# Performance work log

Hardware: AMD Instinct MI355X
Metric: run time of the kernel (lower is better)

Reference implementation:

```python
import jax, jax.numpy as jnp
import numpy as np

B, DIN, H, NACT = 8192, 1025, 1024, 1026
NHEAD = 513  # npatches + STOP
K = 32       # kR = kS


def _make_seq(key, batch, n, k):
    k_idx, k_len = jax.random.split(key)
    # distinct indices per row: top-k of a random permutation
    perm = jnp.argsort(jax.random.uniform(k_idx, (batch, n)), axis=1)[:, :k]
    seq_len = jax.random.randint(k_len, (batch,), 1, k + 1).astype(jnp.int32)
    mask = jnp.arange(k)[None, :] < seq_len[:, None]
    seq_idx = jnp.where(mask, perm, -1).astype(jnp.int32)
    return seq_idx, seq_len


def setup_inputs() -> dict:
    key = jax.random.key(0)
    ks = jax.random.split(key, 8)
    state = jax.random.normal(ks[0], (B, DIN), dtype=jnp.float32)
    W0 = jax.random.normal(ks[1], (DIN, H), dtype=jnp.float32) * (2.0 / DIN) ** 0.5
    b0 = jnp.zeros((H,), jnp.float32)
    W1 = jax.random.normal(ks[2], (H, H), dtype=jnp.float32) * (2.0 / H) ** 0.5
    b1 = jnp.zeros((H,), jnp.float32)
    W2 = jax.random.normal(ks[3], (H, NACT), dtype=jnp.float32) * 0.01
    b2 = jnp.zeros((NACT,), jnp.float32)
    seq_idx_R, seq_len_R = _make_seq(ks[4], B, NHEAD, K)
    seq_idx_S, seq_len_S = _make_seq(ks[5], B, NHEAD, K)
    return {"state": state, "W0": W0, "b0": b0, "W1": W1, "b1": b1,
            "W2": W2, "b2": b2,
            "seq_idx_R": seq_idx_R, "seq_len_R": seq_len_R,
            "seq_idx_S": seq_idx_S, "seq_len_S": seq_len_S}


def _mlp(state, W0, b0, W1, b1, W2, b2):
    h = jax.nn.relu(state @ W0 + b0)
    h = jax.nn.relu(h @ W1 + b1)
    return h @ W2 + b2  # (B, NACT) logits


def _logprob_entropy_wo_replacement(logits, seq_idx, seq_len):
    # Faithful vectorized version of logprob_entropy_wo_replacement_batched.
    bsz, n = logits.shape
    col = jnp.arange(n)[None, :]
    neg_inf = jnp.float32(-jnp.inf)

    def step(carry, xs):
        remaining, logp, ent = carry          # (B,N) bool, (B,), (B,)
        t, idx_t = xs                          # scalar, (B,)
        active = t < seq_len                   # (B,)
        masked_logits = jnp.where(remaining, logits, neg_inf)
        lp = jax.nn.log_softmax(masked_logits, axis=-1)
        p = jnp.exp(lp)
        mp = jnp.where(remaining, p, 0.0)
        mlp_ = jnp.where(remaining, lp, 0.0)
        ent_step = -jnp.sum(mp * mlp_, axis=-1)
        ent = ent + jnp.where(active, ent_step, 0.0)
        valid = active & (idx_t >= 0)
        idx_safe = jnp.where(valid, idx_t, 0)
        g = jnp.take_along_axis(lp, idx_safe[:, None], axis=1)[:, 0]
        logp = logp + jnp.where(valid, g, 0.0)
        hit = (col == idx_safe[:, None]) & valid[:, None]
        remaining = remaining & ~hit
        return (remaining, logp, ent), None

    init = (jnp.ones((bsz, n), bool), jnp.zeros((bsz,), jnp.float32),
            jnp.zeros((bsz,), jnp.float32))
    ts = jnp.arange(seq_idx.shape[1], dtype=jnp.int32)
    (_, logp, ent), _ = jax.lax.scan(step, init, (ts, seq_idx.T))
    return logp, ent


def reference(state, W0, b0, W1, b1, W2, b2,
              seq_idx_R, seq_len_R, seq_idx_S, seq_len_S):
    x = _mlp(state, W0, b0, W1, b1, W2, b2)
    logpR, entR = _logprob_entropy_wo_replacement(x[:, :NHEAD], seq_idx_R, seq_len_R)
    logpS, entS = _logprob_entropy_wo_replacement(x[:, NHEAD:NHEAD + NHEAD], seq_idx_S, seq_len_S)
    # rows: [total logprob, total entropy] as in get_log_prob's (logpR+logpS, entR+entS)
    return jnp.stack([logpR + logpS, entR + entS], axis=0)  # (2, B)
```

## Files before the change

### kernel.cpp

```cpp
#include <hip/hip_runtime.h>
#include <cstdint>
#include <cstddef>

#define BATCH 8192
#define DIN   1025
#define HID   1024
#define NACT  1026
#define NHEAD 513
#define KSEL  32
#define KP0   1088
#define LGN   1024

typedef unsigned short u16;
typedef short bf16x8 __attribute__((ext_vector_type(8)));
typedef float f32x4 __attribute__((ext_vector_type(4)));

__device__ __forceinline__ u16 f2bf(float f) {
  unsigned u = __float_as_uint(f);
  u += 0x7fff + ((u >> 16) & 1);
  return (u16)(u >> 16);
}
__device__ __forceinline__ float bf2f(u16 h) {
  return __uint_as_float((unsigned)h << 16);
}

__device__ __forceinline__ void async_cp16(const u16* g, u16* l) {
  __builtin_amdgcn_global_load_lds((const __attribute__((address_space(1))) void*)g,
                                   (__attribute__((address_space(3))) void*)l,
                                   16, 0, 0);
}

__global__ __launch_bounds__(512) void k_cvt(const float* __restrict__ state,
    const float* __restrict__ W0, const float* __restrict__ W1,
    const float* __restrict__ W2,
    u16* __restrict__ As, u16* __restrict__ W0t, u16* __restrict__ W1t,
    u16* __restrict__ W2t, u16* __restrict__ W2c) {
  const int tid = threadIdx.x;
  const int b = blockIdx.x;
  {
    int i = b * 512 + tid;
    const int QPR = KP0 / 4;
    int r = i / QPR, c4 = (i - r * QPR) * 4;
    const float* src = state + (size_t)r * DIN + c4;
    ushort4 o;
    if (c4 + 3 < DIN) {
      o.x = f2bf(src[0]); o.y = f2bf(src[1]); o.z = f2bf(src[2]); o.w = f2bf(src[3]);
    } else {
      o.x = (c4 + 0 < DIN) ? f2bf(src[0]) : 0;
      o.y = (c4 + 1 < DIN) ? f2bf(src[1]) : 0;
      o.z = (c4 + 2 < DIN) ? f2bf(src[2]) : 0;
      o.w = (c4 + 3 < DIN) ? f2bf(src[3]) : 0;
    }
    *(ushort4*)(As + (size_t)r * KP0 + c4) = o;
  }
  if (b >= 3137) return;
  if (b == 3136) {
    for (int e = tid; e < 2048; e += 512) {
      int j = e >> 10, k = e & 1023;
      W2c[e] = f2bf(W2[(size_t)k * NACT + 1024 + j]);
    }
    return;
  }
  const float* W; u16* Wt; int K, ldW, Kp, tt = b;
  if (tt < 1088)      { W = W0; Wt = W0t; K = DIN; ldW = HID;  Kp = KP0; }
  else if (tt < 2112) { tt -= 1088; W = W1; Wt = W1t; K = HID; ldW = HID;  Kp = HID; }
  else                { tt -= 2112; W = W2; Wt = W2t; K = HID; ldW = NACT; Kp = HID; }
  int n0 = (tt & 31) * 32, k0 = (tt >> 5) * 32;
  __shared__ float tile[32][33];
  const int tx = tid & 31, ty = tid >> 5;
#pragma unroll
  for (int i = 0; i < 32; i += 16) {
    int k = k0 + ty + i;
    tile[ty + i][tx] = (k < K) ? W[(size_t)k * ldW + n0 + tx] : 0.f;
  }
  __syncthreads();
#pragma unroll
  for (int i = 0; i < 32; i += 16)
    Wt[(size_t)(n0 + ty + i) * Kp + k0 + tx] = f2bf(tile[tx][ty + i]);
}

template<bool RELU, int K>
__global__ __launch_bounds__(512, 2)
void gemm256(const u16* __restrict__ A, const u16* __restrict__ Bt,
             const float* __restrict__ bias, u16* __restrict__ Cout, int ldc)
{
  __shared__ __align__(16) u16 lds[65536];

  const int d = blockIdx.x;
  const int wg    = (d & 7) * 16 + (d >> 3);
  const int mtile = wg >> 2;
  const int ntile = wg & 3;
  const size_t bm = (size_t)mtile * 256;
  const size_t bn = (size_t)ntile * 256;

  const int tid  = threadIdx.x;
  const int wave = tid >> 6;
  const int lane = tid & 63;
  const int waveM = wave >> 2, waveN = wave & 3;
  const int lr = lane & 15, lq = lane >> 4;
  const int xr = lr & 7;

  const int row0 = tid >> 3;
  const int g_   = (tid & 7) ^ ((tid >> 3) & 7);
  const u16* gA0 = A  + (bm + row0)       * (size_t)K + g_ * 8;
  const u16* gA1 = A  + (bm + row0 + 64)  * (size_t)K + g_ * 8;
  const u16* gA2 = A  + (bm + row0 + 128) * (size_t)K + g_ * 8;
  const u16* gA3 = A  + (bm + row0 + 192) * (size_t)K + g_ * 8;
  const u16* gB0 = Bt + (bn + row0)       * (size_t)K + g_ * 8;
  const u16* gB1 = Bt + (bn + row0 + 64)  * (size_t)K + g_ * 8;
  const u16* gB2 = Bt + (bn + row0 + 128) * (size_t)K + g_ * 8;
  const u16* gB3 = Bt + (bn + row0 + 192) * (size_t)K + g_ * 8;
  u16* lA = lds + wave * 512;
  u16* lB = lds + 16384 + wave * 512;

  const u16* paA = lds + (waveM * 128 + lr) * 64;
  const u16* paB = lds + 16384 + (waveN * 64 + lr) * 64;
  const int s0 = ( lq      ^ xr) * 8;
  const int s1 = ((4 | lq) ^ xr) * 8;

  f32x4 acc[8][4] = {};
  bf16x8 af[4], ag[4], bfr[4], bgr[4];

  {
    async_cp16(gA0, lA);            async_cp16(gA1, lA + 4096);
    async_cp16(gA2, lA + 8192);     async_cp16(gA3, lA + 12288);
    async_cp16(gB0, lB);            async_cp16(gB1, lB + 4096);
    async_cp16(gB2, lB + 8192);     async_cp16(gB3, lB + 12288);
    asm volatile("s_waitcnt vmcnt(0)" ::: "memory");
    __builtin_amdgcn_s_barrier();
  }

  const int NIT = K / 64;
#pragma unroll 2
  for (int it = 0; it < NIT; ++it) {
    const int bo  = (it & 1) ? 32768 : 0;
    const int bo2 = 32768 - bo;
    const int kn  = (it + 1) * 64;
    const bool pf = (it + 1 < NIT);

#pragma unroll
    for (int nf = 0; nf < 4; ++nf) bfr[nf] = *(const bf16x8*)(paB + bo + nf * 1024 + s0);
#pragma unroll
    for (int mf = 0; mf < 4; ++mf) af[mf]  = *(const bf16x8*)(paA + bo + mf * 1024 + s0);
    if (pf) {
      async_cp16(gA0 + kn, lA + bo2);         async_cp16(gA1 + kn, lA + bo2 + 4096);
      async_cp16(gA2 + kn, lA + bo2 + 8192);  async_cp16(gA3 + kn, lA + bo2 + 12288);
    }
    __builtin_amdgcn_s_barrier();
    asm volatile("s_waitcnt lgkmcnt(0)" ::: "memory");
    __builtin_amdgcn_sched_barrier(0);
    __builtin_amdgcn_s_setprio(1);
#pragma unroll
    for (int mf = 0; mf < 4; ++mf)
#pragma unroll
      for (int nf = 0; nf < 4; ++nf)
        acc[mf][nf] = __builtin_amdgcn_mfma_f32_16x16x32_bf16(af[mf], bfr[nf], acc[mf][nf], 0, 0, 0);
    __builtin_amdgcn_s_setprio(0);
    __builtin_amdgcn_s_barrier();

#pragma unroll
    for (int mf = 0; mf < 4; ++mf) ag[mf] = *(const bf16x8*)(paA + bo + (mf + 4) * 1024 + s0);
    if (pf) {
      async_cp16(gB0 + kn, lB + bo2);         async_cp16(gB1 + kn, lB + bo2 + 4096);
      async_cp16(gB2 + kn, lB + bo2 + 8192);  async_cp16(gB3 + kn, lB + bo2 + 12288);
    }
    __builtin_amdgcn_s_barrier();
    asm volatile("s_waitcnt lgkmcnt(0)" ::: "memory");
    __builtin_amdgcn_sched_barrier(0);
    __builtin_amdgcn_s_setprio(1);
#pragma unroll
    for (int mf = 0; mf < 4; ++mf)
#pragma unroll
      for (int nf = 0; nf < 4; ++nf)
        acc[mf + 4][nf] = __builtin_amdgcn_mfma_f32_16x16x32_bf16(ag[mf], bfr[nf], acc[mf + 4][nf], 0, 0, 0);
    __builtin_amdgcn_s_setprio(0);
    __builtin_amdgcn_s_barrier();

#pragma unroll
    for (int nf = 0; nf < 4; ++nf) bgr[nf] = *(const bf16x8*)(paB + bo + nf * 1024 + s1);
#pragma unroll
    for (int mf = 0; mf < 4; ++mf) af[mf]  = *(const bf16x8*)(paA + bo + mf * 1024 + s1);
    __builtin_amdgcn_s_barrier();
    asm volatile("s_waitcnt lgkmcnt(0)" ::: "memory");
    __builtin_amdgcn_sched_barrier(0);
    __builtin_amdgcn_s_setprio(1);
#pragma unroll
    for (int mf = 0; mf < 4; ++mf)
#pragma unroll
      for (int nf = 0; nf < 4; ++nf)
        acc[mf][nf] = __builtin_amdgcn_mfma_f32_16x16x32_bf16(af[mf], bgr[nf], acc[mf][nf], 0, 0, 0);
    __builtin_amdgcn_s_setprio(0);
    __builtin_amdgcn_s_barrier();

#pragma unroll
    for (int mf = 0; mf < 4; ++mf) ag[mf] = *(const bf16x8*)(paA + bo + (mf + 4) * 1024 + s1);
    __builtin_amdgcn_s_barrier();
    asm volatile("s_waitcnt lgkmcnt(0)" ::: "memory");
    __builtin_amdgcn_sched_barrier(0);
    __builtin_amdgcn_s_setprio(1);
#pragma unroll
    for (int mf = 0; mf < 4; ++mf)
#pragma unroll
      for (int nf = 0; nf < 4; ++nf)
        acc[mf + 4][nf] = __builtin_amdgcn_mfma_f32_16x16x32_bf16(ag[mf], bgr[nf], acc[mf + 4][nf], 0, 0, 0);
    __builtin_amdgcn_s_setprio(0);
    if (pf) asm volatile("s_waitcnt vmcnt(0)" ::: "memory");
    __builtin_amdgcn_s_barrier();
  }

#pragma unroll
  for (int mf = 0; mf < 8; ++mf) {
    size_t rw = bm + waveM * 128 + mf * 16 + lq * 4;
#pragma unroll
    for (int nf = 0; nf < 4; ++nf) {
      int col = (int)bn + waveN * 64 + nf * 16 + lr;
      float bv = bias[col];
#pragma unroll
      for (int r = 0; r < 4; ++r) {
        float v = acc[mf][nf][r] + bv;
        if (RELU) v = fmaxf(v, 0.f);
        Cout[(rw + r) * (size_t)ldc + col] = f2bf(v);
      }
    }
  }
}

__global__ __launch_bounds__(512) void k_sample(const u16* __restrict__ lgts,
    const u16* __restrict__ h2, const u16* __restrict__ W2c,
    const float* __restrict__ b2,
    const int* __restrict__ idxR, const int* __restrict__ lenR,
    const int* __restrict__ idxS, const int* __restrict__ lenS,
    float* __restrict__ out) {
  __shared__ float shf[16];
  const int tid = threadIdx.x;
  const int w = tid >> 6, lane = tid & 63;
  const int grp = w & 1, pair = w >> 1;
  const int row = blockIdx.x * 4 + pair;
  const u16* base = lgts + (size_t)row * LGN + (grp ? NHEAD : 0);
  const int* sidx = (grp ? idxS : idxR) + (size_t)row * KSEL;
  const int slen  = (grp ? lenS : lenR)[row];

  float x1024 = 0.f, x1025 = 0.f;
  if (grp) {
    const bf16x8* hp  = (const bf16x8*)(h2 + (size_t)row * HID + lane * 16);
    const bf16x8* w0p = (const bf16x8*)(W2c + lane * 16);
    const bf16x8* w1p = (const bf16x8*)(W2c + 1024 + lane * 16);
    bf16x8 hv0 = hp[0],  hv1 = hp[1];
    bf16x8 a0  = w0p[0], a1  = w0p[1];
    bf16x8 c0  = w1p[0], c1  = w1p[1];
    float d0 = 0.f, d1 = 0.f;
#pragma unroll
    for (int j = 0; j < 8; ++j) {
      float h0 = bf2f((u16)hv0[j]);
      float h1 = bf2f((u16)hv1[j]);
      d0 += h0 * bf2f((u16)a0[j]) + h1 * bf2f((u16)a1[j]);
      d1 += h0 * bf2f((u16)c0[j]) + h1 * bf2f((u16)c1[j]);
    }
#pragma unroll
    for (int dd = 32; dd; dd >>= 1) { d0 += __shfl_xor(d0, dd, 64); d1 += __shfl_xor(d1, dd, 64); }
    x1024 = d0 + b2[1024];
    x1025 = d1 + b2[1025];
  }

  const u16* chunk = lgts + (size_t)row * LGN + (grp ? 512 : 0) + lane * 8;
  bf16x8 raw = *(const bf16x8*)chunk;
  float v[8];
#pragma unroll
  for (int j = 0; j < 8; ++j) v[j] = bf2f((u16)raw[j]);
  if (grp && lane == 0) v[0] = -3.4e38f;

  float xa = -3.4e38f; int has_xa = 0;
  if (!grp && lane == 0)  { xa = bf2f(base[512]); has_xa = 1; }
  if (grp  && lane == 63) { xa = x1024;           has_xa = 1; }
  if (grp  && lane == 0)  { xa = x1025;           has_xa = 1; }

  float m = -3.4e38f;
#pragma unroll
  for (int j = 0; j < 8; ++j) m = fmaxf(m, v[j]);
  if (has_xa) m = fmaxf(m, xa);
#pragma unroll
  for (int dd = 32; dd; dd >>= 1) m = fmaxf(m, __shfl_xor(m, dd, 64));

  float S = 0.f, T = 0.f;
#pragma unroll
  for (int j = 0; j < 8; ++j) {
    float e = __expf(v[j] - m);
    S += e; T += e * v[j];
  }
  if (has_xa) { float e = __expf(xa - m); S += e; T += e * xa; }
#pragma unroll
  for (int dd = 32; dd; dd >>= 1) { S += __shfl_xor(S, dd, 64); T += __shfl_xor(T, dd, 64); }

  float e = 0.f, ex = 0.f, xt = 0.f;
  int active = (lane < KSEL) && (lane < slen);
  int valid = 0;
  if (active) {
    int id = sidx[lane];
    if (id >= 0) {
      valid = 1;
      if (grp && id >= 511) xt = (id == 511) ? x1024 : x1025;
      else                  xt = bf2f(base[id]);
      e  = __expf(xt - m);
      ex = e * xt;
    }
  }
  float pe = e, pex = ex;
#pragma unroll
  for (int dd = 1; dd < 32; dd <<= 1) {
    float qa = __shfl_up(pe, dd, 64);
    float qb = __shfl_up(pex, dd, 64);
    if (lane >= dd) { pe += qa; pex += qb; }
  }
  float lp = 0.f, en = 0.f;
  if (active) {
    float St = S - (pe - e);
    float Tt = T - (pex - ex);
    float logZ = m + __logf(St);
    en = logZ - Tt / St;
    if (valid) lp = xt - logZ;
  }
#pragma unroll
  for (int dd = 32; dd; dd >>= 1) { lp += __shfl_xor(lp, dd, 64); en += __shfl_xor(en, dd, 64); }

  if (lane == 0) { shf[w * 2] = lp; shf[w * 2 + 1] = en; }
  __syncthreads();
  if (lane == 0 && grp == 0) {
    out[row]         = shf[pair * 4] + shf[pair * 4 + 2];
    out[BATCH + row] = shf[pair * 4 + 1] + shf[pair * 4 + 3];
  }
}

extern "C" void kernel_launch(void* const* d_in, const int* in_sizes, int n_in,
                              void* d_out, int out_size, void* d_ws, size_t ws_size,
                              hipStream_t stream) {
  (void)in_sizes; (void)n_in; (void)out_size; (void)ws_size;
  const float* state = (const float*)d_in[0];
  const float* W0 = (const float*)d_in[1];
  const float* b0 = (const float*)d_in[2];
  const float* W1 = (const float*)d_in[3];
  const float* b1 = (const float*)d_in[4];
  const float* W2 = (const float*)d_in[5];
  const float* b2 = (const float*)d_in[6];
  const int* idxR = (const int*)d_in[7];
  const int* lenR = (const int*)d_in[8];
  const int* idxS = (const int*)d_in[9];
  const int* lenS = (const int*)d_in[10];
  float* out = (float*)d_out;

  char* ws = (char*)d_ws;
  size_t off = 0;
  auto alloc = [&](size_t bytes) -> char* {
    char* p = ws + off;
    off = (off + bytes + 255) & ~(size_t)255;
    return p;
  };
  u16* As   = (u16*)alloc((size_t)BATCH * KP0 * 2);
  u16* W0t  = (u16*)alloc((size_t)HID * KP0 * 2);
  u16* W1t  = (u16*)alloc((size_t)HID * HID * 2);
  u16* W2t  = (u16*)alloc((size_t)HID * LGN * 2);
  u16* W2c  = (u16*)alloc((size_t)2 * 1024 * 2);
  u16* h1   = (u16*)alloc((size_t)BATCH * HID * 2);
  u16* h2   = (u16*)alloc((size_t)BATCH * HID * 2);
  u16* lgts = (u16*)alloc((size_t)BATCH * LGN * 2);

  k_cvt<<<4352, 512, 0, stream>>>(state, W0, W1, W2, As, W0t, W1t, W2t, W2c);

  gemm256<true,  KP0><<<128, 512, 0, stream>>>(As, W0t, b0, h1,   HID);
  gemm256<true,  HID><<<128, 512, 0, stream>>>(h1, W1t, b1, h2,   HID);
  gemm256<false, HID><<<128, 512, 0, stream>>>(h2, W2t, b2, lgts, LGN);

  k_sample<<<2048, 512, 0, stream>>>(lgts, h2, W2c, b2, idxR, lenR, idxS, lenS, out);
}
```

Measured before the change: 216.5 us.

## Use 256x128 GEMM tiles with triple-buffered LDS prefetch and 256 blocks

Shrinks the GEMM output tile from 256x256 to 256x128, so each launch uses 256 workgroups instead of 128 and fills more of the MI355X's compute units. The shared-memory pipeline moves from double to triple buffering, with stages prefetched two iterations ahead and partial vmcnt waits. The aim is better CU occupancy and more latency hiding for the async global-to-LDS copies. In exchange, each tile reuses loaded data less, so operand traffic per FLOP rises, and the tile uses more LDS.

```diff
diff --git a/kernel.cpp b/kernel.cpp
--- a/kernel.cpp
+++ b/kernel.cpp
@@ -80,23 +80,23 @@
 }
 
 template<bool RELU, int K>
-__global__ __launch_bounds__(512, 2)
-void gemm256(const u16* __restrict__ A, const u16* __restrict__ Bt,
+__global__ __launch_bounds__(512, 1)
+void gemm_bt(const u16* __restrict__ A, const u16* __restrict__ Bt,
              const float* __restrict__ bias, u16* __restrict__ Cout, int ldc)
 {
-  __shared__ __align__(16) u16 lds[65536];
+  __shared__ __align__(16) u16 lds[73728];
 
   const int d = blockIdx.x;
-  const int wg    = (d & 7) * 16 + (d >> 3);
-  const int mtile = wg >> 2;
-  const int ntile = wg & 3;
+  const int wg    = (d & 7) * 32 + (d >> 3);
+  const int mtile = wg >> 3;
+  const int ntile = wg & 7;
   const size_t bm = (size_t)mtile * 256;
-  const size_t bn = (size_t)ntile * 256;
+  const size_t bn = (size_t)ntile * 128;
 
   const int tid  = threadIdx.x;
   const int wave = tid >> 6;
   const int lane = tid & 63;
-  const int waveM = wave >> 2, waveN = wave & 3;
+  const int waveM = wave >> 1, waveN = wave & 1;
   const int lr = lane & 15, lq = lane >> 4;
   const int xr = lr & 7;
 
@@ -108,43 +108,44 @@
   const u16* gA3 = A  + (bm + row0 + 192) * (size_t)K + g_ * 8;
   const u16* gB0 = Bt + (bn + row0)       * (size_t)K + g_ * 8;
   const u16* gB1 = Bt + (bn + row0 + 64)  * (size_t)K + g_ * 8;
-  const u16* gB2 = Bt + (bn + row0 + 128) * (size_t)K + g_ * 8;
-  const u16* gB3 = Bt + (bn + row0 + 192) * (size_t)K + g_ * 8;
-  u16* lA = lds + wave * 512;
-  u16* lB = lds + 16384 + wave * 512;
-
-  const u16* paA = lds + (waveM * 128 + lr) * 64;
-  const u16* paB = lds + 16384 + (waveN * 64 + lr) * 64;
+
+  auto stage = [&](int k0, int wb) {
+    u16* a = lds + wb * 24576 + wave * 512;
+    u16* b = a + 16384;
+    async_cp16(gA0 + k0, a);
+    async_cp16(gA1 + k0, a + 4096);
+    async_cp16(gA2 + k0, a + 8192);
+    async_cp16(gA3 + k0, a + 12288);
+    async_cp16(gB0 + k0, b);
+    async_cp16(gB1 + k0, b + 4096);
+  };
+
+  const int offA = (waveM * 64 + lr) * 64;
+  const int offB = 16384 + (waveN * 64 + lr) * 64;
   const int s0 = ( lq      ^ xr) * 8;
   const int s1 = ((4 | lq) ^ xr) * 8;
 
-  f32x4 acc[8][4] = {};
-  bf16x8 af[4], ag[4], bfr[4], bgr[4];
-
-  {
-    async_cp16(gA0, lA);            async_cp16(gA1, lA + 4096);
-    async_cp16(gA2, lA + 8192);     async_cp16(gA3, lA + 12288);
-    async_cp16(gB0, lB);            async_cp16(gB1, lB + 4096);
-    async_cp16(gB2, lB + 8192);     async_cp16(gB3, lB + 12288);
-    asm volatile("s_waitcnt vmcnt(0)" ::: "memory");
-    __builtin_amdgcn_s_barrier();
-  }
+  f32x4 acc[4][4] = {};
+  bf16x8 af[4], bfr[4];
 
   const int NIT = K / 64;
-#pragma unroll 2
-  for (int it = 0; it < NIT; ++it) {
-    const int bo  = (it & 1) ? 32768 : 0;
-    const int bo2 = 32768 - bo;
-    const int kn  = (it + 1) * 64;
-    const bool pf = (it + 1 < NIT);
-
-#pragma unroll
-    for (int nf = 0; nf < 4; ++nf) bfr[nf] = *(const bf16x8*)(paB + bo + nf * 1024 + s0);
-#pragma unroll
-    for (int mf = 0; mf < 4; ++mf) af[mf]  = *(const bf16x8*)(paA + bo + mf * 1024 + s0);
+  stage(0, 0);
+  stage(64, 1);
+  asm volatile("s_waitcnt vmcnt(6)" ::: "memory");
+  __builtin_amdgcn_s_barrier();
+
+  int rb = 0;
+  for (int t = 0; t < NIT; ++t) {
+    const int ro = rb * 24576;
+    const bool pf = (t + 2 < NIT);
+
+#pragma unroll
+    for (int nf = 0; nf < 4; ++nf) bfr[nf] = *(const bf16x8*)(lds + ro + offB + nf * 1024 + s0);
+#pragma unroll
+    for (int mf = 0; mf < 4; ++mf) af[mf]  = *(const bf16x8*)(lds + ro + offA + mf * 1024 + s0);
     if (pf) {
-      async_cp16(gA0 + kn, lA + bo2);         async_cp16(gA1 + kn, lA + bo2 + 4096);
-      async_cp16(gA2 + kn, lA + bo2 + 8192);  async_cp16(gA3 + kn, lA + bo2 + 12288);
+      int wb = rb - 1; if (wb < 0) wb = 2;
+      stage((t + 2) * 64, wb);
     }
     __builtin_amdgcn_s_barrier();
     asm volatile("s_waitcnt lgkmcnt(0)" ::: "memory");
@@ -159,11 +160,9 @@
     __builtin_amdgcn_s_barrier();
 
 #pragma unroll
-    for (int mf = 0; mf < 4; ++mf) ag[mf] = *(const bf16x8*)(paA + bo + (mf + 4) * 1024 + s0);
-    if (pf) {
-      async_cp16(gB0 + kn, lB + bo2);         async_cp16(gB1 + kn, lB + bo2 + 4096);
-      async_cp16(gB2 + kn, lB + bo2 + 8192);  async_cp16(gB3 + kn, lB + bo2 + 12288);
-    }
+    for (int nf = 0; nf < 4; ++nf) bfr[nf] = *(const bf16x8*)(lds + ro + offB + nf * 1024 + s1);
+#pragma unroll
+    for (int mf = 0; mf < 4; ++mf) af[mf]  = *(const bf16x8*)(lds + ro + offA + mf * 1024 + s1);
     __builtin_amdgcn_s_barrier();
     asm volatile("s_waitcnt lgkmcnt(0)" ::: "memory");
     __builtin_amdgcn_sched_barrier(0);
@@ -172,45 +171,18 @@
     for (int mf = 0; mf < 4; ++mf)
 #pragma unroll
       for (int nf = 0; nf < 4; ++nf)
-        acc[mf + 4][nf] = __builtin_amdgcn_mfma_f32_16x16x32_bf16(ag[mf], bfr[nf], acc[mf + 4][nf], 0, 0, 0);
+        acc[mf][nf] = __builtin_amdgcn_mfma_f32_16x16x32_bf16(af[mf], bfr[nf], acc[mf][nf], 0, 0, 0);
     __builtin_amdgcn_s_setprio(0);
+    if (pf)               asm volatile("s_waitcnt vmcnt(6)" ::: "memory");
+    else if (t + 1 < NIT) asm volatile("s_waitcnt vmcnt(0)" ::: "memory");
     __builtin_amdgcn_s_barrier();
 
-#pragma unroll
-    for (int nf = 0; nf < 4; ++nf) bgr[nf] = *(const bf16x8*)(paB + bo + nf * 1024 + s1);
-#pragma unroll
-    for (int mf = 0; mf < 4; ++mf) af[mf]  = *(const bf16x8*)(paA + bo + mf * 1024 + s1);
-    __builtin_amdgcn_s_barrier();
-    asm volatile("s_waitcnt lgkmcnt(0)" ::: "memory");
-    __builtin_amdgcn_sched_barrier(0);
-    __builtin_amdgcn_s_setprio(1);
-#pragma unroll
-    for (int mf = 0; mf < 4; ++mf)
-#pragma unroll
-      for (int nf = 0; nf < 4; ++nf)
-        acc[mf][nf] = __builtin_amdgcn_mfma_f32_16x16x32_bf16(af[mf], bgr[nf], acc[mf][nf], 0, 0, 0);
-    __builtin_amdgcn_s_setprio(0);
-    __builtin_amdgcn_s_barrier();
-
-#pragma unroll
-    for (int mf = 0; mf < 4; ++mf) ag[mf] = *(const bf16x8*)(paA + bo + (mf + 4) * 1024 + s1);
-    __builtin_amdgcn_s_barrier();
-    asm volatile("s_waitcnt lgkmcnt(0)" ::: "memory");
-    __builtin_amdgcn_sched_barrier(0);
-    __builtin_amdgcn_s_setprio(1);
-#pragma unroll
-    for (int mf = 0; mf < 4; ++mf)
-#pragma unroll
-      for (int nf = 0; nf < 4; ++nf)
-        acc[mf + 4][nf] = __builtin_amdgcn_mfma_f32_16x16x32_bf16(ag[mf], bgr[nf], acc[mf + 4][nf], 0, 0, 0);
-    __builtin_amdgcn_s_setprio(0);
-    if (pf) asm volatile("s_waitcnt vmcnt(0)" ::: "memory");
-    __builtin_amdgcn_s_barrier();
-  }
-
-#pragma unroll
-  for (int mf = 0; mf < 8; ++mf) {
-    size_t rw = bm + waveM * 128 + mf * 16 + lq * 4;
+    rb = (rb == 2) ? 0 : rb + 1;
+  }
+
+#pragma unroll
+  for (int mf = 0; mf < 4; ++mf) {
+    size_t rw = bm + waveM * 64 + mf * 16 + lq * 4;
 #pragma unroll
     for (int nf = 0; nf < 4; ++nf) {
       int col = (int)bn + waveN * 64 + nf * 16 + lr;
@@ -365,9 +337,9 @@
 
   k_cvt<<<4352, 512, 0, stream>>>(state, W0, W1, W2, As, W0t, W1t, W2t, W2c);
 
-  gemm256<true,  KP0><<<128, 512, 0, stream>>>(As, W0t, b0, h1,   HID);
-  gemm256<true,  HID><<<128, 512, 0, stream>>>(h1, W1t, b1, h2,   HID);
-  gemm256<false, HID><<<128, 512, 0, stream>>>(h2, W2t, b2, lgts, LGN);
+  gemm_bt<true,  KP0><<<256, 512, 0, stream>>>(As, W0t, b0, h1,   HID);
+  gemm_bt<true,  HID><<<256, 512, 0, stream>>>(h1, W1t, b1, h2,   HID);
+  gemm_bt<false, HID><<<256, 512, 0, stream>>>(h2, W2t, b2, lgts, LGN);
 
   k_sample<<<2048, 512, 0, stream>>>(lgts, h2, W2c, b2, idxR, lenR, idxS, lenS, out);
 }
```

Measured after the change: 185.0 us. -14.5%, faster.
